# Performance work log

Measured on AMD Instinct MI355X. Metric: run time of the kernel, lower is better.

Reference implementation:

```python
import jax, jax.numpy as jnp
import numpy as np
from jax import lax

K = 8
SCALE = 100.0

# ---- straight-through binarizers (match torch custom Functions) ----
@jax.custom_vjp
def bin_w(x):
    return jnp.sign(x)

def _bin_w_fwd(x):
    return jnp.sign(x), None

def _bin_w_bwd(_, g):
    return (g,)  # identity STE

bin_w.defvjp(_bin_w_fwd, _bin_w_bwd)

@jax.custom_vjp
def bin_a(x):
    return jnp.sign(x)

def _bin_a_fwd(x):
    return jnp.sign(x), x

def _bin_a_bwd(x, g):
    return (g * jnp.clip(2.0 - jnp.abs(2.0 * x), 0.0, None),)

bin_a.defvjp(_bin_a_fwd, _bin_a_bwd)

# ---- SDP sampling with custom backward (grad_z scaled by sqrt(scale)) ----
@jax.custom_vjp
def sdp(m, z, rv):
    # m: (N,), z: (K,N), rv: (1,K) -> w: (N,)
    return (rv @ z)[0] + m

def _sdp_fwd(m, z, rv):
    return (rv @ z)[0] + m, rv

def _sdp_bwd(rv, g):
    grad_m = g
    grad_z = (rv.T @ g[None, :]) * np.sqrt(SCALE)  # (K,N)
    return (grad_m, grad_z, jnp.zeros_like(rv))

sdp.defvjp(_sdp_fwd, _sdp_bwd)

def _forward(x, M, Z, alpha, rv):
    N = M.size
    m = M.reshape(N)          # (N,)
    z = Z.reshape(K, N)       # (K,N)
    # no_grad normalization of m,z data: value changes, gradient passes through identity
    A = m * m + jnp.sum(z * z, axis=0) / SCALE
    inv = lax.rsqrt(A)
    m_used = m + lax.stop_gradient(m * inv - m)
    z_used = z + lax.stop_gradient(z * inv - z)
    w = sdp(m_used, z_used, rv)               # (N,)
    bw = bin_w(w).reshape(M.shape)            # (O,I,3,3) in {-1,+1}
    ba = bin_a(x)                             # (B,C,H,W) in {-1,+1}
    out = lax.conv_general_dilated(
        ba, bw, window_strides=(1, 1), padding=((1, 1), (1, 1)),
        dimension_numbers=('NCHW', 'OIHW', 'NCHW'))
    return out * alpha  # alpha (O,1,1) broadcasts over (B,O,H,W)

def setup_inputs() -> dict:
    key = jax.random.key(0)
    k1, k2, k3, k4, k5 = jax.random.split(key, 5)
    x = jax.random.normal(k1, (64, 256, 28, 28), dtype=jnp.float32)
    M = jax.random.normal(k2, (256, 256, 3, 3), dtype=jnp.float32)
    Z = jax.random.normal(k3, (8, 256, 256, 3, 3), dtype=jnp.float32)
    alpha = jax.random.uniform(k4, (256, 1, 1), dtype=jnp.float32)
    rv = jax.random.normal(k5, (1, 8), dtype=jnp.float32) * np.float32(1.0 / np.sqrt(SCALE))
    return {"x": x, "M": M, "Z": Z, "alpha": alpha, "rv": rv}

def reference(x, M, Z, alpha, rv):
    return _forward(x, M, Z, alpha, rv)
```

## Files before the change

kernel.cpp:

```cpp
#include <hip/hip_runtime.h>
#include <stdint.h>

typedef unsigned int uint32;

#define BB 64
#define CC 256
#define OO 256
#define HH 28
#define WW 28
#define HWP 784
#define NWT 589824

__global__ __launch_bounds__(256) void pack_x_kernel(
    const float* __restrict__ x, uint32* __restrict__ apack) {
  int p = blockIdx.x * 256 + threadIdx.x;
  int j = blockIdx.y;
  int b = blockIdx.z;
  if (p >= HWP) return;
  const float* xp = x + ((size_t)(b * CC + j * 32) * HWP) + p;
  uint32 m = 0;
#pragma unroll
  for (int cc = 0; cc < 32; ++cc) {
    float v = xp[(size_t)cc * HWP];
    m |= ((uint32)(v > 0.0f)) << cc;
  }
  apack[((size_t)b * HWP + p) * 8 + j] = m;
}

__global__ __launch_bounds__(256) void pack_w_kernel(
    const float* __restrict__ M, const float* __restrict__ Z,
    const float* __restrict__ rv, uint32* __restrict__ wpack) {
  __shared__ float sacc[576];
  const int o = blockIdx.x;
  const int jh = blockIdx.y;
  const int tid = threadIdx.x;
  const size_t base = (size_t)o * 2304 + (size_t)jh * 576;

  float r[8];
#pragma unroll
  for (int k = 0; k < 8; ++k) r[k] = rv[k];

#pragma unroll
  for (int ii = 0; ii < 3; ++ii) {
    int i = tid + ii * 256;
    if (i < 576) {
      float s = M[base + i];
#pragma unroll
      for (int k = 0; k < 8; ++k) s += r[k] * Z[(size_t)k * NWT + base + i];
      sacc[i] = s;
    }
  }
  __syncthreads();

  if (tid < 18) {
    int tap = tid % 9;
    int jj = tid / 9;
    uint32 m = 0;
#pragma unroll
    for (int cc = 0; cc < 32; ++cc) {
      float v = sacc[(jj * 32 + cc) * 9 + tap];
      m |= ((uint32)(v > 0.0f)) << cc;
    }
    wpack[(o * 9 + tap) * 8 + jh * 2 + jj] = m;
  }
}

__global__ __launch_bounds__(256, 3) void conv_kernel(
    const uint32* __restrict__ apack, const uint32* __restrict__ wpack,
    const float* __restrict__ alpha, float* __restrict__ out) {
  __shared__ float res[OO][WW + 1];

  const int h = blockIdx.x;
  const int b = blockIdx.y;
  const int o = threadIdx.x;

  uint32 wr[9][8];
  const uint4* wp = (const uint4*)(wpack + (size_t)o * 72);
#pragma unroll
  for (int t = 0; t < 9; ++t) {
    uint4 lo = wp[t * 2];
    uint4 hi = wp[t * 2 + 1];
    wr[t][0] = lo.x; wr[t][1] = lo.y; wr[t][2] = lo.z; wr[t][3] = lo.w;
    wr[t][4] = hi.x; wr[t][5] = hi.y; wr[t][6] = hi.z; wr[t][7] = hi.w;
  }
#pragma unroll
  for (int t = 0; t < 9; ++t)
#pragma unroll
    for (int j = 0; j < 8; ++j) asm volatile("" : "+v"(wr[t][j]));

  const float av = alpha[o];

  for (int w = 0; w < WW; ++w) {
    int cnt = 0;
    int nv = 0;
#pragma unroll
    for (int dh = 0; dh < 3; ++dh) {
      int hh = h + dh - 1;
      if ((unsigned)hh >= (unsigned)HH) continue;
#pragma unroll
      for (int dw = 0; dw < 3; ++dw) {
        int ww = w + dw - 1;
        if ((unsigned)ww >= (unsigned)WW) continue;
        ++nv;
        const uint4* ap =
            (const uint4*)(apack + ((size_t)b * HWP + hh * WW + ww) * 8);
        uint4 a0 = ap[0];
        uint4 a1 = ap[1];
        const uint32* wt = wr[dh * 3 + dw];
        cnt += __popc(a0.x ^ wt[0]) + __popc(a0.y ^ wt[1]) +
               __popc(a0.z ^ wt[2]) + __popc(a0.w ^ wt[3]) +
               __popc(a1.x ^ wt[4]) + __popc(a1.y ^ wt[5]) +
               __popc(a1.z ^ wt[6]) + __popc(a1.w ^ wt[7]);
      }
    }
    res[o][w] = av * (float)(256 * nv - 2 * cnt);
  }
  __syncthreads();

  const size_t base = (size_t)b * OO * HWP + (size_t)h * WW;
  for (int idx = threadIdx.x; idx < OO * WW; idx += 256) {
    int oo = idx / WW;
    int ww = idx - oo * WW;
    out[base + (size_t)oo * HWP + ww] = res[oo][ww];
  }
}

extern "C" void kernel_launch(void* const* d_in, const int* in_sizes, int n_in,
                              void* d_out, int out_size, void* d_ws,
                              size_t ws_size, hipStream_t stream) {
  const float* x     = (const float*)d_in[0];
  const float* M     = (const float*)d_in[1];
  const float* Z     = (const float*)d_in[2];
  const float* alpha = (const float*)d_in[3];
  const float* rv    = (const float*)d_in[4];
  float* out = (float*)d_out;

  uint32* apack = (uint32*)d_ws;
  uint32* wpack = (uint32*)((char*)d_ws + 1605632);

  pack_x_kernel<<<dim3(4, 8, BB), 256, 0, stream>>>(x, apack);
  pack_w_kernel<<<dim3(256, 4), 256, 0, stream>>>(M, Z, rv, wpack);
  conv_kernel<<<dim3(HH, BB), 256, 0, stream>>>(apack, wpack, alpha, out);
}
```

Before: 193.1 us.

## Restructure binary conv: pixel-per-thread with LDS activation slab and zero-padded borders

Replaces the output-channel-per-thread conv with a layout where each thread owns one output pixel and loops over 64 output channels, reading activations from a zero-padded LDS slab and weights as wave-uniform scalar loads. Border handling is moved into a precomputed per-channel, per-border-class correction table built by a new small kernel, so the inner loop has no branches. Output stores become coalesced along pixels, which removes the LDS transpose stage. In exchange the padded slab adds wasted XOR/popcount work on border taps, there is one extra kernel launch, and the last tile is partially idle.

```diff
diff --git a/kernel.cpp b/kernel.cpp
--- a/kernel.cpp
+++ b/kernel.cpp
@@ -10,6 +10,10 @@
 #define WW 28
 #define HWP 784
 #define NWT 589824
+
+#define SROWS 12
+#define SCOLS 30
+#define SLAB_DW (SROWS * SCOLS * 8)
 
 __global__ __launch_bounds__(256) void pack_x_kernel(
     const float* __restrict__ x, uint32* __restrict__ apack) {
@@ -65,63 +69,103 @@
   }
 }
 
-__global__ __launch_bounds__(256, 3) void conv_kernel(
-    const uint32* __restrict__ apack, const uint32* __restrict__ wpack,
-    const float* __restrict__ alpha, float* __restrict__ out) {
-  __shared__ float res[OO][WW + 1];
-
-  const int h = blockIdx.x;
-  const int b = blockIdx.y;
-  const int o = threadIdx.x;
-
-  uint32 wr[9][8];
-  const uint4* wp = (const uint4*)(wpack + (size_t)o * 72);
+__global__ __launch_bounds__(256) void ptab_kernel(
+    const uint32* __restrict__ wpack, const float* __restrict__ alpha,
+    float* __restrict__ ptabA, float* __restrict__ ptabM) {
+  int o = threadIdx.x;
+  const uint32* wt = wpack + (size_t)o * 72;
+  int pt[9];
 #pragma unroll
   for (int t = 0; t < 9; ++t) {
-    uint4 lo = wp[t * 2];
-    uint4 hi = wp[t * 2 + 1];
-    wr[t][0] = lo.x; wr[t][1] = lo.y; wr[t][2] = lo.z; wr[t][3] = lo.w;
-    wr[t][4] = hi.x; wr[t][5] = hi.y; wr[t][6] = hi.z; wr[t][7] = hi.w;
+    int s = 0;
+#pragma unroll
+    for (int j = 0; j < 8; ++j) s += __popc(wt[t * 8 + j]);
+    pt[t] = s;
   }
+  int row0 = pt[0] + pt[1] + pt[2], row2 = pt[6] + pt[7] + pt[8];
+  int col0 = pt[0] + pt[3] + pt[6], col2 = pt[2] + pt[5] + pt[8];
+  float a = alpha[o];
+  const int nv[9] = {4, 6, 4, 6, 9, 6, 4, 6, 4};
+  int S[9];
+  S[0] = row0 + col0 - pt[0]; S[1] = row0; S[2] = row0 + col2 - pt[2];
+  S[3] = col0;                S[4] = 0;    S[5] = col2;
+  S[6] = row2 + col0 - pt[6]; S[7] = row2; S[8] = row2 + col2 - pt[8];
 #pragma unroll
-  for (int t = 0; t < 9; ++t)
-#pragma unroll
-    for (int j = 0; j < 8; ++j) asm volatile("" : "+v"(wr[t][j]));
+  for (int c = 0; c < 9; ++c)
+    ptabA[o * 9 + c] = a * (float)(256 * nv[c] + 2 * S[c]);
+  ptabM[o] = -2.0f * a;
+}
 
-  const float av = alpha[o];
+__global__ __launch_bounds__(256, 4) void conv_kernel(
+    const uint32* __restrict__ apack, const uint32* __restrict__ wpack,
+    const float* __restrict__ ptabA, const float* __restrict__ ptabM,
+    float* __restrict__ out) {
+  __shared__ uint32 slab[SLAB_DW];
+  __shared__ float atab[64 * 9];
 
-  for (int w = 0; w < WW; ++w) {
-    int cnt = 0;
-    int nv = 0;
-#pragma unroll
-    for (int dh = 0; dh < 3; ++dh) {
-      int hh = h + dh - 1;
-      if ((unsigned)hh >= (unsigned)HH) continue;
-#pragma unroll
-      for (int dw = 0; dw < 3; ++dw) {
-        int ww = w + dw - 1;
-        if ((unsigned)ww >= (unsigned)WW) continue;
-        ++nv;
-        const uint4* ap =
-            (const uint4*)(apack + ((size_t)b * HWP + hh * WW + ww) * 8);
-        uint4 a0 = ap[0];
-        uint4 a1 = ap[1];
-        const uint32* wt = wr[dh * 3 + dw];
-        cnt += __popc(a0.x ^ wt[0]) + __popc(a0.y ^ wt[1]) +
-               __popc(a0.z ^ wt[2]) + __popc(a0.w ^ wt[3]) +
-               __popc(a1.x ^ wt[4]) + __popc(a1.y ^ wt[5]) +
-               __popc(a1.z ^ wt[6]) + __popc(a1.w ^ wt[7]);
-      }
+  const int tile = blockIdx.x;
+  const int og = blockIdx.y;
+  const int b = blockIdx.z;
+  const int tid = threadIdx.x;
+
+  const int p0 = tile * 256;
+  const int r0 = (p0 / 28) - 1;
+
+  for (int i = tid; i < 576; i += 256) atab[i] = ptabA[og * 576 + i];
+
+  for (int i = tid; i < SLAB_DW / 4; i += 256)
+    ((uint4*)slab)[i] = make_uint4(0, 0, 0, 0);
+  __syncthreads();
+
+  for (int q = tid; q < 672; q += 256) {
+    int row = q / 56;
+    int c16 = q - row * 56;
+    int r = r0 + row;
+    if (r >= 0 && r < HH) {
+      const uint4* src =
+          (const uint4*)(apack + ((size_t)(b * HWP + r * WW) * 8)) + c16;
+      ((uint4*)slab)[(row * SCOLS + 1) * 2 + c16] = *src;
     }
-    res[o][w] = av * (float)(256 * nv - 2 * cnt);
   }
   __syncthreads();
 
-  const size_t base = (size_t)b * OO * HWP + (size_t)h * WW;
-  for (int idx = threadIdx.x; idx < OO * WW; idx += 256) {
-    int oo = idx / WW;
-    int ww = idx - oo * WW;
-    out[base + (size_t)oo * HWP + ww] = res[oo][ww];
+  if (p0 + (tid & ~63) >= HWP) return;
+
+  const int p = p0 + tid;
+  const bool active = p < HWP;
+  const int h = p / 28;
+  const int w = p - h * 28;
+  const int hc = (h == 0) ? 0 : (h == 27 ? 2 : 1);
+  const int wc = (w == 0) ? 0 : (w == 27 ? 2 : 1);
+  const int cls = hc * 3 + wc;
+  const int abase = ((h - r0 - 1) * SCOLS + w) * 32;
+  const char* sbase = (const char*)slab + abase;
+
+  const size_t outbase = ((size_t)b * OO + og * 64) * HWP + p;
+
+  for (int oi = 0; oi < 64; ++oi) {
+    const int o = og * 64 + oi;
+    const int wo = __builtin_amdgcn_readfirstlane(o * 72);
+    const uint32* wt = wpack + wo;
+    const float m = ptabM[o];
+
+    int total = 0;
+#pragma unroll
+    for (int dh = 0; dh < 3; ++dh) {
+#pragma unroll
+      for (int dw = 0; dw < 3; ++dw) {
+        const uint4* sp = (const uint4*)(sbase + (dh * SCOLS + dw) * 32);
+        uint4 a0 = sp[0];
+        uint4 a1 = sp[1];
+        const uint32* wtt = wt + (dh * 3 + dw) * 8;
+        total += __popc(a0.x ^ wtt[0]) + __popc(a0.y ^ wtt[1]) +
+                 __popc(a0.z ^ wtt[2]) + __popc(a0.w ^ wtt[3]) +
+                 __popc(a1.x ^ wtt[4]) + __popc(a1.y ^ wtt[5]) +
+                 __popc(a1.z ^ wtt[6]) + __popc(a1.w ^ wtt[7]);
+      }
+    }
+    float res = fmaf(m, (float)total, atab[oi * 9 + cls]);
+    if (active) out[outbase + (size_t)oi * HWP] = res;
   }
 }
 
@@ -137,8 +181,12 @@
 
   uint32* apack = (uint32*)d_ws;
   uint32* wpack = (uint32*)((char*)d_ws + 1605632);
+  float* ptabA  = (float*)((char*)d_ws + 1679360);
+  float* ptabM  = (float*)((char*)d_ws + 1688576);
 
   pack_x_kernel<<<dim3(4, 8, BB), 256, 0, stream>>>(x, apack);
   pack_w_kernel<<<dim3(256, 4), 256, 0, stream>>>(M, Z, rv, wpack);
-  conv_kernel<<<dim3(HH, BB), 256, 0, stream>>>(apack, wpack, alpha, out);
+  ptab_kernel<<<dim3(1), 256, 0, stream>>>(wpack, alpha, ptabA, ptabM);
+  conv_kernel<<<dim3(4, 4, BB), 256, 0, stream>>>(apack, wpack, ptabA, ptabM,
+                                                  out);
 }
```

After: 225.3 us. 1.17x slower.
